# Optimization experiments

Hardware: AMD Instinct MI355X
Metric: run time of the kernel (lower is better)

## Reference

```python
import jax, jax.numpy as jnp
import numpy as np

BINARY_K = 64  # self.binary_k


def setup_inputs() -> dict:
    key = jax.random.key(0)
    ks = jax.random.split(key, 8)
    R, N, D, H = 8, 128, 512, 256
    obj_feats = jax.random.normal(ks[0], (R, N, D), dtype=jnp.float32)
    geo_feats = jax.random.normal(ks[1], (R, N, N, D), dtype=jnp.float32) * 0.1
    mask = jnp.ones((N, N), dtype=jnp.float32)
    mask = mask.at[jnp.arange(N), jnp.arange(N)].set(0.0)  # zero diagonal, as in forward()
    s1 = 1.0 / np.sqrt(D)
    s2 = 1.0 / np.sqrt(H)
    return {
        "obj_feats": obj_feats,
        "geo_feats": geo_feats,
        "mask": mask,
        "w1a": jax.random.normal(ks[2], (D, H), dtype=jnp.float32) * s1,
        "b1a": jnp.zeros((H,), dtype=jnp.float32),
        "w2a": jax.random.normal(ks[3], (H, 1), dtype=jnp.float32) * s2,
        "b2a": jnp.zeros((1,), dtype=jnp.float32),
        "w1b": jax.random.normal(ks[4], (D, H), dtype=jnp.float32) * s1,
        "b1b": jnp.zeros((H,), dtype=jnp.float32),
        "w2b": jax.random.normal(ks[5], (H, 1), dtype=jnp.float32) * s2,
        "b2b": jnp.zeros((1,), dtype=jnp.float32),
    }


def reference(obj_feats, geo_feats, mask, w1a, b1a, w2a, b2a, w1b, b1b, w2b, b2b):
    # pair_aware_perbatch (dropout = identity in eval mode)
    R, N, D = obj_feats.shape
    k = min(BINARY_K, N * N)

    # pairwise outer-product features + geometric features: [R, N, N, D]
    obj2obj = obj_feats[:, None, :, :] * obj_feats[:, :, None, :] + geo_feats

    # re_clf1 MLP scorer: D -> D/2 -> 1
    h = jax.nn.relu(jnp.einsum('rijd,dh->rijh', obj2obj, w1a) + b1a)
    logits = jnp.einsum('rijh,h->rij', h, w2a[:, 0]) + b2a[0]     # [R, N, N]
    o2o_logits = logits.reshape(R, N * N).sum(axis=0) / R          # [N*N]

    pair_probs = jax.nn.sigmoid(o2o_logits) * mask.ravel()
    _, topk_inds = jax.lax.top_k(pair_probs, k)                    # [k]

    # averaged pair features, gather topk
    a_obj2obj = obj2obj.reshape(R, N * N, D).sum(axis=0) / R       # [N*N, D]
    pair_feats = a_obj2obj[topk_inds]                              # [k, D]

    # pair-of-pair outer product + second MLP scorer
    p2p = pair_feats[None, :, :] * pair_feats[:, None, :]          # [k, k, D]
    h2 = jax.nn.relu(jnp.einsum('ijd,dh->ijh', p2p, w1b) + b1b)
    p2p_logits = jnp.einsum('ijh,h->ij', h2, w2b[:, 0]) + b2b[0]   # [k, k]

    return o2o_logits.reshape(N, N), p2p_logits, topk_inds
```

## Files before the change

### kernel.cpp

```cpp
#include <hip/hip_runtime.h>
#include <math.h>

typedef unsigned int u32;
typedef unsigned long long u64;
typedef unsigned short u16;
typedef short bf16x8 __attribute__((ext_vector_type(8)));
typedef float f32x4 __attribute__((ext_vector_type(4)));

#define RR 8
#define NN 128
#define DD 512
#define HH 256
#define KTOP 64
#define NCAND 256
#define NSEL 128

#define WS_LOGITS_OFF 0
#define WS_CAND_OFF   65536
#define WS_EXACT_OFF  66560
#define WS_CNT_OFF    67584
#define WS_TOPK_OFF   67600
#define WS_PF_OFF     67856
#define WS_WH_OFF     198928
#define WS_WL_OFF     461072

__device__ __forceinline__ u16 bf16rne(float x) {
    union { float f; u32 u; } v; v.f = x;
    u32 r = (v.u + 0x7fffu + ((v.u >> 16) & 1u)) >> 16;
    return (u16)r;
}
__device__ __forceinline__ float bf16tof(u16 h) {
    union { float f; u32 u; } v; v.u = ((u32)h) << 16; return v.f;
}
__device__ __forceinline__ u32 f32sort(float x) {
    union { float f; u32 u; } v; v.f = x;
    return v.u ^ ((v.u & 0x80000000u) ? 0xFFFFFFFFu : 0x80000000u);
}

__global__ __launch_bounds__(256) void k0_splitW(const float* __restrict__ W1,
                                                 u16* __restrict__ wh, u16* __restrict__ wl)
{
    const int kc = blockIdx.x;
    const int h  = threadIdx.x;
    const int swz = (h >> 1) & 3;
    u16 rh[32], rl[32];
#pragma unroll
    for (int kk = 0; kk < 32; ++kk) {
        float a = W1[(size_t)(kc * 32 + kk) * HH + h];
        u16 hi = bf16rne(a);
        float lo = a - bf16tof(hi);
        rh[kk] = hi; rl[kk] = bf16rne(lo);
    }
    const size_t base = (size_t)kc * 8192 + (size_t)h * 32;
#pragma unroll
    for (int q = 0; q < 4; ++q) {
        uint4 ph, pl;
        ph.x = (u32)rh[q*8+0] | ((u32)rh[q*8+1] << 16);
        ph.y = (u32)rh[q*8+2] | ((u32)rh[q*8+3] << 16);
        ph.z = (u32)rh[q*8+4] | ((u32)rh[q*8+5] << 16);
        ph.w = (u32)rh[q*8+6] | ((u32)rh[q*8+7] << 16);
        pl.x = (u32)rl[q*8+0] | ((u32)rl[q*8+1] << 16);
        pl.y = (u32)rl[q*8+2] | ((u32)rl[q*8+3] << 16);
        pl.z = (u32)rl[q*8+4] | ((u32)rl[q*8+5] << 16);
        pl.w = (u32)rl[q*8+6] | ((u32)rl[q*8+7] << 16);
        const int qs = (q ^ swz) * 8;
        *(uint4*)&wh[base + qs] = ph;
        *(uint4*)&wl[base + qs] = pl;
    }
}

__global__ __launch_bounds__(256, 2) void k1_pair_mfma(
    const float* __restrict__ obj, const float* __restrict__ geo,
    const u16* __restrict__ wh, const u16* __restrict__ wl,
    const float* __restrict__ b1, const float* __restrict__ w2,
    float* __restrict__ logits_acc)
{
    const int jb = blockIdx.x, i = blockIdx.y, r = blockIdx.z;
    const int j0 = jb * 64;
    const int tid = threadIdx.x;
    const int lane = tid & 63, wv = tid >> 6;
    const int l15 = lane & 15, quad = lane >> 4;
    const int fsl = (quad ^ ((l15 >> 1) & 3)) * 8;

    __shared__ float sObjI[DD];
    __shared__ __align__(16) u16 sAh[64 * 32], sAl[64 * 32];
    __shared__ __align__(16) u16 sBh[256 * 32], sBl[256 * 32];

    const float* objI = obj + (size_t)(r * NN + i) * DD;
    for (int t = tid; t < DD; t += 256) sObjI[t] = objI[t];

    f32x4 acc[4][4];
#pragma unroll
    for (int mt = 0; mt < 4; ++mt)
#pragma unroll
        for (int nt = 0; nt < 4; ++nt) acc[mt][nt] = (f32x4){0.f, 0.f, 0.f, 0.f};

    const float* geoB = geo + ((size_t)(r * NN + i) * NN + j0) * DD;
    const float* objJ = obj + (size_t)(r * NN + j0) * DD;

    const int aj = tid >> 2;
    const int ak = (tid & 3) * 8;
    const int asl = ((tid & 3) ^ ((aj >> 1) & 3)) * 8;

    for (int kc = 0; kc < 16; ++kc) {
        const int k0 = kc * 32;
        __syncthreads();
        {
            const char* gh = (const char*)(wh + (size_t)kc * 8192);
            const char* gl = (const char*)(wl + (size_t)kc * 8192);
#pragma unroll
            for (int p = 0; p < 4; ++p) {
                const int off = (wv * 4 + p) * 1024;
                __builtin_amdgcn_global_load_lds(
                    (const __attribute__((address_space(1))) u32*)(gh + off + lane * 16),
                    (__attribute__((address_space(3))) u32*)((char*)sBh + off), 16, 0, 0);
                __builtin_amdgcn_global_load_lds(
                    (const __attribute__((address_space(1))) u32*)(gl + off + lane * 16),
                    (__attribute__((address_space(3))) u32*)((char*)sBl + off), 16, 0, 0);
            }
        }
        {
            float4 g0 = *(const float4*)(geoB + (size_t)aj * DD + k0 + ak);
            float4 g1 = *(const float4*)(geoB + (size_t)aj * DD + k0 + ak + 4);
            float4 o0 = *(const float4*)(objJ + (size_t)aj * DD + k0 + ak);
            float4 o1 = *(const float4*)(objJ + (size_t)aj * DD + k0 + ak + 4);
            float a[8];
            a[0] = fmaf(sObjI[k0+ak+0], o0.x, g0.x);
            a[1] = fmaf(sObjI[k0+ak+1], o0.y, g0.y);
            a[2] = fmaf(sObjI[k0+ak+2], o0.z, g0.z);
            a[3] = fmaf(sObjI[k0+ak+3], o0.w, g0.w);
            a[4] = fmaf(sObjI[k0+ak+4], o1.x, g1.x);
            a[5] = fmaf(sObjI[k0+ak+5], o1.y, g1.y);
            a[6] = fmaf(sObjI[k0+ak+6], o1.z, g1.z);
            a[7] = fmaf(sObjI[k0+ak+7], o1.w, g1.w);
            u16 hs[8], ls[8];
#pragma unroll
            for (int q = 0; q < 8; ++q) {
                hs[q] = bf16rne(a[q]);
                ls[q] = bf16rne(a[q] - bf16tof(hs[q]));
            }
            uint4 ph, pl;
            ph.x = (u32)hs[0] | ((u32)hs[1] << 16); ph.y = (u32)hs[2] | ((u32)hs[3] << 16);
            ph.z = (u32)hs[4] | ((u32)hs[5] << 16); ph.w = (u32)hs[6] | ((u32)hs[7] << 16);
            pl.x = (u32)ls[0] | ((u32)ls[1] << 16); pl.y = (u32)ls[2] | ((u32)ls[3] << 16);
            pl.z = (u32)ls[4] | ((u32)ls[5] << 16); pl.w = (u32)ls[6] | ((u32)ls[7] << 16);
            *(uint4*)&sAh[aj * 32 + asl] = ph;
            *(uint4*)&sAl[aj * 32 + asl] = pl;
        }
        __syncthreads();
        bf16x8 Bh[4], Bl[4], Ah[4], Al[4];
#pragma unroll
        for (int nt = 0; nt < 4; ++nt) {
            const int row = wv * 64 + nt * 16 + l15;
            Bh[nt] = *(const bf16x8*)&sBh[row * 32 + fsl];
            Bl[nt] = *(const bf16x8*)&sBl[row * 32 + fsl];
        }
#pragma unroll
        for (int mt = 0; mt < 4; ++mt) {
            const int row = mt * 16 + l15;
            Ah[mt] = *(const bf16x8*)&sAh[row * 32 + fsl];
            Al[mt] = *(const bf16x8*)&sAl[row * 32 + fsl];
        }
#pragma unroll
        for (int mt = 0; mt < 4; ++mt)
#pragma unroll
            for (int nt = 0; nt < 4; ++nt) {
                acc[mt][nt] = __builtin_amdgcn_mfma_f32_16x16x32_bf16(Ah[mt], Bh[nt], acc[mt][nt], 0, 0, 0);
                acc[mt][nt] = __builtin_amdgcn_mfma_f32_16x16x32_bf16(Ah[mt], Bl[nt], acc[mt][nt], 0, 0, 0);
                acc[mt][nt] = __builtin_amdgcn_mfma_f32_16x16x32_bf16(Al[mt], Bh[nt], acc[mt][nt], 0, 0, 0);
            }
    }
    float pr[4][4];
#pragma unroll
    for (int mt = 0; mt < 4; ++mt)
#pragma unroll
        for (int t = 0; t < 4; ++t) pr[mt][t] = 0.f;
#pragma unroll
    for (int nt = 0; nt < 4; ++nt) {
        const int h = wv * 64 + nt * 16 + l15;
        const float bb = b1[h], w = w2[h];
#pragma unroll
        for (int mt = 0; mt < 4; ++mt)
#pragma unroll
            for (int t = 0; t < 4; ++t)
                pr[mt][t] += fmaxf(acc[mt][nt][t] + bb, 0.f) * w;
    }
#pragma unroll
    for (int mt = 0; mt < 4; ++mt)
#pragma unroll
        for (int t = 0; t < 4; ++t) {
            float v = pr[mt][t];
            v += __shfl_xor(v, 1); v += __shfl_xor(v, 2);
            v += __shfl_xor(v, 4); v += __shfl_xor(v, 8);
            if (l15 == 0)
                atomicAdd(&logits_acc[i * NN + j0 + mt * 16 + quad * 4 + t], v);
        }
}

__global__ __launch_bounds__(1024) void k2_hist(
    const float* __restrict__ logits_acc, const float* __restrict__ mask,
    const float* __restrict__ b2a, float* __restrict__ out,
    int* __restrict__ cand, int* __restrict__ cnt_out)
{
    __shared__ u32 hist[16 * 256];
    __shared__ u32 sum1[256];
    __shared__ int sB1, sRem, sT16;
    __shared__ u32 sCnt;
    const int t = threadIdx.x;
    const int hb = (t >> 6) << 8;
    for (int b = t; b < 16 * 256; b += 1024) hist[b] = 0;
    if (t == 0) sCnt = 0;
    __syncthreads();
    const float bias = b2a[0];
    u32 skey[16];
#pragma unroll
    for (int e = 0; e < 16; ++e) {
        const int idx = e * 1024 + t;
        const float lg = logits_acc[idx] * 0.125f + bias;
        out[idx] = lg;
        u32 s = f32sort(lg);
        if (mask[idx] == 0.f) s = 0;
        skey[e] = s;
        atomicAdd(&hist[hb + (s >> 24)], 1u);
    }
    __syncthreads();
    if (t < 256) {
        u32 s = 0;
#pragma unroll
        for (int c = 0; c < 16; ++c) s += hist[c * 256 + t];
        sum1[t] = s;
    }
    __syncthreads();
    if (t == 0) {
        u32 cum = 0; int b = 255;
        for (; b > 0; --b) { u32 c = sum1[b]; if (cum + c >= (u32)NSEL) break; cum += c; }
        sB1 = b; sRem = NSEL - (int)cum;
    }
    __syncthreads();
    const int B1 = sB1;
    for (int b = t; b < 16 * 256; b += 1024) hist[b] = 0;
    __syncthreads();
#pragma unroll
    for (int e = 0; e < 16; ++e) {
        const u32 s = skey[e];
        if ((int)(s >> 24) == B1) atomicAdd(&hist[hb + ((s >> 16) & 0xFF)], 1u);
    }
    __syncthreads();
    if (t < 256) {
        u32 s = 0;
#pragma unroll
        for (int c = 0; c < 16; ++c) s += hist[c * 256 + t];
        sum1[t] = s;
    }
    __syncthreads();
    if (t == 0) {
        const int rem = sRem; u32 cum = 0; int b = 255;
        for (; b > 0; --b) { cum += sum1[b]; if ((int)cum >= rem) break; }
        sT16 = (B1 << 8) | b;
    }
    __syncthreads();
    const u32 T16 = (u32)sT16;
#pragma unroll
    for (int e = 0; e < 16; ++e) {
        const u32 s = skey[e];
        if (s != 0 && (s >> 16) >= T16) {
            const u32 pos = atomicAdd(&sCnt, 1u);
            if (pos < (u32)NCAND) cand[pos] = e * 1024 + t;
        }
    }
    __syncthreads();
    if (t == 0) *cnt_out = (int)(sCnt < (u32)NCAND ? sCnt : (u32)NCAND);
}

__global__ __launch_bounds__(256) void k5_exact(
    const float* __restrict__ obj, const float* __restrict__ geo,
    const float* __restrict__ W1, const float* __restrict__ b1,
    const float* __restrict__ w2, const float* __restrict__ b2a,
    const int* __restrict__ cand, const int* __restrict__ cnt_ptr,
    float* __restrict__ exact)
{
    const int c = blockIdx.x;
    if (c >= *cnt_ptr) { if (threadIdx.x == 0) exact[c] = -1e30f; return; }
    const int idx = cand[c];
    const int i = idx >> 7, j = idx & 127;
    const int t = threadIdx.x;
    __shared__ float sA[RR][DD];
    __shared__ float sRed[4];
    for (int f = t; f < RR * DD; f += 256) {
        const int r = f >> 9, k = f & 511;
        sA[r][k] = fmaf(obj[(size_t)(r * NN + i) * DD + k],
                        obj[(size_t)(r * NN + j) * DD + k],
                        geo[((size_t)(r * NN + i) * NN + j) * DD + k]);
    }
    __syncthreads();
    float hv[RR];
#pragma unroll
    for (int r = 0; r < RR; ++r) hv[r] = 0.f;
#pragma unroll 4
    for (int k = 0; k < DD; ++k) {
        const float w = W1[(size_t)k * HH + t];
#pragma unroll
        for (int r = 0; r < RR; ++r) hv[r] = fmaf(sA[r][k], w, hv[r]);
    }
    const float bb = b1[t], wv2 = w2[t];
    float p = 0.f;
#pragma unroll
    for (int r = 0; r < RR; ++r) p += fmaxf(hv[r] + bb, 0.f) * wv2;
#pragma unroll
    for (int off = 1; off < 64; off <<= 1) p += __shfl_xor(p, off);
    if ((t & 63) == 0) sRed[t >> 6] = p;
    __syncthreads();
    if (t == 0) exact[c] = (sRed[0] + sRed[1] + sRed[2] + sRed[3]) * 0.125f + b2a[0];
}

__global__ __launch_bounds__(256) void k_sort(
    const float* __restrict__ exact, const int* __restrict__ cand,
    float* __restrict__ out, int* __restrict__ topk)
{
    __shared__ u64 sKey[NCAND];
    const int t = threadIdx.x;
    {
        const float lg = exact[t];
        u32 ps = 0; u32 idx = 0x7FFFFFFFu;
        if (lg > -1e29f) {
            const float p = 1.f / (1.f + expf(-lg));
            ps = f32sort(p);
            idx = (u32)cand[t];
        }
        sKey[t] = ((u64)ps << 32) | (u64)(0xFFFFFFFFu - idx);
    }
    for (int k = 2; k <= NCAND; k <<= 1)
        for (int j = k >> 1; j > 0; j >>= 1) {
            __syncthreads();
            const int ixj = t ^ j;
            if (ixj > t) {
                const u64 a = sKey[t], b = sKey[ixj];
                if (((t & k) == 0) ? (a < b) : (a > b)) { sKey[t] = b; sKey[ixj] = a; }
            }
        }
    __syncthreads();
    if (t < KTOP) {
        const u32 idx = 0xFFFFFFFFu - (u32)(sKey[t] & 0xFFFFFFFFull);
        topk[t] = (int)idx;
        out[20480 + t] = (float)idx;
    }
}

__global__ __launch_bounds__(256) void k3_gather(
    const float* __restrict__ obj, const float* __restrict__ geo,
    const int* __restrict__ ws_topk, float* __restrict__ pf)
{
    const int tix = blockIdx.x;
    const int idx = ws_topk[tix];
    const int i = idx >> 7, j = idx & 127;
    for (int dd = threadIdx.x; dd < DD; dd += 256) {
        float s = 0.f;
#pragma unroll
        for (int r = 0; r < RR; ++r) {
            const float oi = obj[(size_t)(r * NN + i) * DD + dd];
            const float oj = obj[(size_t)(r * NN + j) * DD + dd];
            const float g  = geo[((size_t)(r * NN + i) * NN + j) * DD + dd];
            s += oi * oj + g;
        }
        pf[tix * DD + dd] = s * 0.125f;
    }
}

__global__ __launch_bounds__(256) void k4_p2p(
    const float* __restrict__ pf, const float* __restrict__ W1,
    const float* __restrict__ b1, const float* __restrict__ w2,
    const float* __restrict__ b2, float* __restrict__ out)
{
    const int a = blockIdx.x;
    const int tid = threadIdx.x;
    const int tx = tid & 15, ty = tid >> 4;

    __shared__ float sPfA[DD];
    __shared__ __align__(16) float sA[32][68];
    __shared__ __align__(16) float sB[32][HH];

    const float* pfA = pf + (size_t)a * DD;
    for (int t = tid; t < DD; t += 256) sPfA[t] = pfA[t];

    float acc[4][16];
#pragma unroll
    for (int m = 0; m < 4; ++m)
#pragma unroll
        for (int n = 0; n < 16; ++n) acc[m][n] = 0.f;

    for (int kc = 0; kc < 16; ++kc) {
        const int k0 = kc * 32;
        __syncthreads();
#pragma unroll
        for (int p = 0; p < 8; ++p) {
            const int f = tid + p * 256;
            const int kk = f >> 6, c = (f & 63) << 2;
            *(float4*)&sB[kk][c] = *(const float4*)&W1[(size_t)(k0 + kk) * HH + c];
        }
#pragma unroll
        for (int p = 0; p < 2; ++p) {
            const int f = tid + p * 256;
            const int j = f >> 3, kk = (f & 7) << 2;
            float4 o = *(const float4*)(pf + (size_t)j * DD + k0 + kk);
            sA[kk + 0][j] = sPfA[k0 + kk + 0] * o.x;
            sA[kk + 1][j] = sPfA[k0 + kk + 1] * o.y;
            sA[kk + 2][j] = sPfA[k0 + kk + 2] * o.z;
            sA[kk + 3][j] = sPfA[k0 + kk + 3] * o.w;
        }
        __syncthreads();
#pragma unroll 8
        for (int kk = 0; kk < 32; ++kk) {
            float4 a4 = *(const float4*)&sA[kk][ty << 2];
            float av[4] = {a4.x, a4.y, a4.z, a4.w};
#pragma unroll
            for (int n4 = 0; n4 < 4; ++n4) {
                float4 b4 = *(const float4*)&sB[kk][(n4 << 6) + (tx << 2)];
                float bv[4] = {b4.x, b4.y, b4.z, b4.w};
#pragma unroll
                for (int m = 0; m < 4; ++m)
#pragma unroll
                    for (int c = 0; c < 4; ++c)
                        acc[m][(n4 << 2) + c] = fmaf(av[m], bv[c], acc[m][(n4 << 2) + c]);
            }
        }
    }
    const float b20 = b2[0];
    float pr[4] = {0.f, 0.f, 0.f, 0.f};
#pragma unroll
    for (int n4 = 0; n4 < 4; ++n4)
#pragma unroll
        for (int c = 0; c < 4; ++c) {
            const int h = (n4 << 6) + (tx << 2) + c;
            const float bb = b1[h], w = w2[h];
#pragma unroll
            for (int m = 0; m < 4; ++m)
                pr[m] += fmaxf(acc[m][(n4 << 2) + c] + bb, 0.f) * w;
        }
#pragma unroll
    for (int m = 0; m < 4; ++m) {
        pr[m] += __shfl_xor(pr[m], 1); pr[m] += __shfl_xor(pr[m], 2);
        pr[m] += __shfl_xor(pr[m], 4); pr[m] += __shfl_xor(pr[m], 8);
        if (tx == 0)
            out[16384 + a * 64 + (ty << 2) + m] = pr[m] + b20;
    }
}

extern "C" void kernel_launch(void* const* d_in, const int* in_sizes, int n_in,
                              void* d_out, int out_size, void* d_ws, size_t ws_size,
                              hipStream_t stream) {
    const float* obj  = (const float*)d_in[0];
    const float* geo  = (const float*)d_in[1];
    const float* mask = (const float*)d_in[2];
    const float* w1a  = (const float*)d_in[3];
    const float* b1a  = (const float*)d_in[4];
    const float* w2a  = (const float*)d_in[5];
    const float* b2a  = (const float*)d_in[6];
    const float* w1b  = (const float*)d_in[7];
    const float* b1b  = (const float*)d_in[8];
    const float* w2b  = (const float*)d_in[9];
    const float* b2b  = (const float*)d_in[10];
    float* out = (float*)d_out;

    char* ws = (char*)d_ws;
    float* ws_logits = (float*)(ws + WS_LOGITS_OFF);
    int*   ws_cand   = (int*)  (ws + WS_CAND_OFF);
    float* ws_exact  = (float*)(ws + WS_EXACT_OFF);
    int*   ws_cnt    = (int*)  (ws + WS_CNT_OFF);
    int*   ws_topk   = (int*)  (ws + WS_TOPK_OFF);
    float* ws_pf     = (float*)(ws + WS_PF_OFF);
    u16*   ws_wh     = (u16*)  (ws + WS_WH_OFF);
    u16*   ws_wl     = (u16*)  (ws + WS_WL_OFF);

    hipMemsetAsync(ws_logits, 0, 16384 * sizeof(float), stream);

    k0_splitW<<<16, 256, 0, stream>>>(w1a, ws_wh, ws_wl);
    k1_pair_mfma<<<dim3(2, NN, RR), 256, 0, stream>>>(obj, geo, ws_wh, ws_wl, b1a, w2a, ws_logits);
    k2_hist<<<1, 1024, 0, stream>>>(ws_logits, mask, b2a, out, ws_cand, ws_cnt);
    k5_exact<<<NCAND, 256, 0, stream>>>(obj, geo, w1a, b1a, w2a, b2a, ws_cand, ws_cnt, ws_exact);
    k_sort<<<1, 256, 0, stream>>>(ws_exact, ws_cand, out, ws_topk);
    k3_gather<<<KTOP, 256, 0, stream>>>(obj, geo, ws_topk, ws_pf);
    k4_p2p<<<KTOP, 256, 0, stream>>>(ws_pf, w1b, b1b, w2b, b2b, out);
}
```

Before: 636.8 us.

## Port p2p scorer to split-bf16 MFMA, fuse sort with gather, fold memset

The second MLP GEMM (k4_p2p) moves from FP32 FMA tiles to bf16 MFMA using a hi/lo split (four MFMAs per tile) to keep near-fp32 accuracy. W1b is split into hi/lo inside the kernel on every chunk. The single-block sort is merged with the top-k gather: each of 64 blocks redundantly sorts and then gathers its own row, which removes one launch. The logits memset is folded into an extra block of the weight-split kernel, and an unroll factor in k5_exact is raised. Together these cut launch count and FMA-bound GEMM time, at the cost of redundant sort work and repeated weight conversion in every block.

```diff
diff --git a/kernel.cpp b/kernel.cpp
--- a/kernel.cpp
+++ b/kernel.cpp
@@ -38,8 +38,15 @@
 }
 
 __global__ __launch_bounds__(256) void k0_splitW(const float* __restrict__ W1,
-                                                 u16* __restrict__ wh, u16* __restrict__ wl)
+                                                 u16* __restrict__ wh, u16* __restrict__ wl,
+                                                 float* __restrict__ logits)
 {
+    if (blockIdx.x == 16) {
+        float4 z = {0.f, 0.f, 0.f, 0.f};
+        for (int t = threadIdx.x; t < 4096; t += 256)
+            ((float4*)logits)[t] = z;
+        return;
+    }
     const int kc = blockIdx.x;
     const int h  = threadIdx.x;
     const int swz = (h >> 1) & 3;
@@ -296,7 +303,7 @@
     float hv[RR];
 #pragma unroll
     for (int r = 0; r < RR; ++r) hv[r] = 0.f;
-#pragma unroll 4
+#pragma unroll 8
     for (int k = 0; k < DD; ++k) {
         const float w = W1[(size_t)k * HH + t];
 #pragma unroll
@@ -313,9 +320,10 @@
     if (t == 0) exact[c] = (sRed[0] + sRed[1] + sRed[2] + sRed[3]) * 0.125f + b2a[0];
 }
 
-__global__ __launch_bounds__(256) void k_sort(
+__global__ __launch_bounds__(256) void k_sortgather(
     const float* __restrict__ exact, const int* __restrict__ cand,
-    float* __restrict__ out, int* __restrict__ topk)
+    const float* __restrict__ obj, const float* __restrict__ geo,
+    float* __restrict__ out, float* __restrict__ pf)
 {
     __shared__ u64 sKey[NCAND];
     const int t = threadIdx.x;
@@ -339,21 +347,14 @@
             }
         }
     __syncthreads();
-    if (t < KTOP) {
-        const u32 idx = 0xFFFFFFFFu - (u32)(sKey[t] & 0xFFFFFFFFull);
-        topk[t] = (int)idx;
-        out[20480 + t] = (float)idx;
-    }
-}
-
-__global__ __launch_bounds__(256) void k3_gather(
-    const float* __restrict__ obj, const float* __restrict__ geo,
-    const int* __restrict__ ws_topk, float* __restrict__ pf)
-{
     const int tix = blockIdx.x;
-    const int idx = ws_topk[tix];
+    if (tix == 0 && t < KTOP) {
+        const u32 oidx = 0xFFFFFFFFu - (u32)(sKey[t] & 0xFFFFFFFFull);
+        out[20480 + t] = (float)oidx;
+    }
+    const int idx = (int)(0xFFFFFFFFu - (u32)(sKey[tix] & 0xFFFFFFFFull));
     const int i = idx >> 7, j = idx & 127;
-    for (int dd = threadIdx.x; dd < DD; dd += 256) {
+    for (int dd = t; dd < DD; dd += 256) {
         float s = 0.f;
 #pragma unroll
         for (int r = 0; r < RR; ++r) {
@@ -373,76 +374,131 @@
 {
     const int a = blockIdx.x;
     const int tid = threadIdx.x;
-    const int tx = tid & 15, ty = tid >> 4;
+    const int lane = tid & 63, wv = tid >> 6;
+    const int l15 = lane & 15, quad = lane >> 4;
+    const int fsl = (quad ^ ((l15 >> 1) & 3)) * 8;
 
     __shared__ float sPfA[DD];
-    __shared__ __align__(16) float sA[32][68];
-    __shared__ __align__(16) float sB[32][HH];
+    __shared__ __align__(16) u16 sAh[64 * 32], sAl[64 * 32];
+    __shared__ __align__(16) u16 sBh[256 * 32], sBl[256 * 32];
+    __shared__ float sRed[4][64];
 
     const float* pfA = pf + (size_t)a * DD;
     for (int t = tid; t < DD; t += 256) sPfA[t] = pfA[t];
 
-    float acc[4][16];
-#pragma unroll
-    for (int m = 0; m < 4; ++m)
-#pragma unroll
-        for (int n = 0; n < 16; ++n) acc[m][n] = 0.f;
+    f32x4 acc[4][4];
+#pragma unroll
+    for (int mt = 0; mt < 4; ++mt)
+#pragma unroll
+        for (int nt = 0; nt < 4; ++nt) acc[mt][nt] = (f32x4){0.f, 0.f, 0.f, 0.f};
+
+    const int aj = tid >> 2;
+    const int ak = (tid & 3) * 8;
+    const int asl = ((tid & 3) ^ ((aj >> 1) & 3)) * 8;
+    const int swzB = (tid >> 1) & 3;
 
     for (int kc = 0; kc < 16; ++kc) {
         const int k0 = kc * 32;
         __syncthreads();
-#pragma unroll
-        for (int p = 0; p < 8; ++p) {
-            const int f = tid + p * 256;
-            const int kk = f >> 6, c = (f & 63) << 2;
-            *(float4*)&sB[kk][c] = *(const float4*)&W1[(size_t)(k0 + kk) * HH + c];
-        }
-#pragma unroll
-        for (int p = 0; p < 2; ++p) {
-            const int f = tid + p * 256;
-            const int j = f >> 3, kk = (f & 7) << 2;
-            float4 o = *(const float4*)(pf + (size_t)j * DD + k0 + kk);
-            sA[kk + 0][j] = sPfA[k0 + kk + 0] * o.x;
-            sA[kk + 1][j] = sPfA[k0 + kk + 1] * o.y;
-            sA[kk + 2][j] = sPfA[k0 + kk + 2] * o.z;
-            sA[kk + 3][j] = sPfA[k0 + kk + 3] * o.w;
+        {
+            u16 rh[32], rl[32];
+#pragma unroll
+            for (int kk = 0; kk < 32; ++kk) {
+                float w = W1[(size_t)(k0 + kk) * HH + tid];
+                u16 hi = bf16rne(w);
+                rh[kk] = hi; rl[kk] = bf16rne(w - bf16tof(hi));
+            }
+#pragma unroll
+            for (int q = 0; q < 4; ++q) {
+                uint4 ph, pl;
+                ph.x = (u32)rh[q*8+0] | ((u32)rh[q*8+1] << 16);
+                ph.y = (u32)rh[q*8+2] | ((u32)rh[q*8+3] << 16);
+                ph.z = (u32)rh[q*8+4] | ((u32)rh[q*8+5] << 16);
+                ph.w = (u32)rh[q*8+6] | ((u32)rh[q*8+7] << 16);
+                pl.x = (u32)rl[q*8+0] | ((u32)rl[q*8+1] << 16);
+                pl.y = (u32)rl[q*8+2] | ((u32)rl[q*8+3] << 16);
+                pl.z = (u32)rl[q*8+4] | ((u32)rl[q*8+5] << 16);
+                pl.w = (u32)rl[q*8+6] | ((u32)rl[q*8+7] << 16);
+                const int qs = (q ^ swzB) * 8;
+                *(uint4*)&sBh[tid * 32 + qs] = ph;
+                *(uint4*)&sBl[tid * 32 + qs] = pl;
+            }
+        }
+        {
+            float4 p0 = *(const float4*)(pf + (size_t)aj * DD + k0 + ak);
+            float4 p1 = *(const float4*)(pf + (size_t)aj * DD + k0 + ak + 4);
+            float av[8];
+            av[0] = sPfA[k0+ak+0] * p0.x; av[1] = sPfA[k0+ak+1] * p0.y;
+            av[2] = sPfA[k0+ak+2] * p0.z; av[3] = sPfA[k0+ak+3] * p0.w;
+            av[4] = sPfA[k0+ak+4] * p1.x; av[5] = sPfA[k0+ak+5] * p1.y;
+            av[6] = sPfA[k0+ak+6] * p1.z; av[7] = sPfA[k0+ak+7] * p1.w;
+            u16 hs[8], ls[8];
+#pragma unroll
+            for (int q = 0; q < 8; ++q) {
+                hs[q] = bf16rne(av[q]);
+                ls[q] = bf16rne(av[q] - bf16tof(hs[q]));
+            }
+            uint4 ph, pl;
+            ph.x = (u32)hs[0] | ((u32)hs[1] << 16); ph.y = (u32)hs[2] | ((u32)hs[3] << 16);
+            ph.z = (u32)hs[4] | ((u32)hs[5] << 16); ph.w = (u32)hs[6] | ((u32)hs[7] << 16);
+            pl.x = (u32)ls[0] | ((u32)ls[1] << 16); pl.y = (u32)ls[2] | ((u32)ls[3] << 16);
+            pl.z = (u32)ls[4] | ((u32)ls[5] << 16); pl.w = (u32)ls[6] | ((u32)ls[7] << 16);
+            *(uint4*)&sAh[aj * 32 + asl] = ph;
+            *(uint4*)&sAl[aj * 32 + asl] = pl;
         }
         __syncthreads();
-#pragma unroll 8
-        for (int kk = 0; kk < 32; ++kk) {
-            float4 a4 = *(const float4*)&sA[kk][ty << 2];
-            float av[4] = {a4.x, a4.y, a4.z, a4.w};
-#pragma unroll
-            for (int n4 = 0; n4 < 4; ++n4) {
-                float4 b4 = *(const float4*)&sB[kk][(n4 << 6) + (tx << 2)];
-                float bv[4] = {b4.x, b4.y, b4.z, b4.w};
-#pragma unroll
-                for (int m = 0; m < 4; ++m)
-#pragma unroll
-                    for (int c = 0; c < 4; ++c)
-                        acc[m][(n4 << 2) + c] = fmaf(av[m], bv[c], acc[m][(n4 << 2) + c]);
-            }
-        }
-    }
-    const float b20 = b2[0];
-    float pr[4] = {0.f, 0.f, 0.f, 0.f};
-#pragma unroll
-    for (int n4 = 0; n4 < 4; ++n4)
-#pragma unroll
-        for (int c = 0; c < 4; ++c) {
-            const int h = (n4 << 6) + (tx << 2) + c;
-            const float bb = b1[h], w = w2[h];
-#pragma unroll
-            for (int m = 0; m < 4; ++m)
-                pr[m] += fmaxf(acc[m][(n4 << 2) + c] + bb, 0.f) * w;
-        }
-#pragma unroll
-    for (int m = 0; m < 4; ++m) {
-        pr[m] += __shfl_xor(pr[m], 1); pr[m] += __shfl_xor(pr[m], 2);
-        pr[m] += __shfl_xor(pr[m], 4); pr[m] += __shfl_xor(pr[m], 8);
-        if (tx == 0)
-            out[16384 + a * 64 + (ty << 2) + m] = pr[m] + b20;
-    }
+        bf16x8 Bh[4], Bl[4], Ah[4], Al[4];
+#pragma unroll
+        for (int nt = 0; nt < 4; ++nt) {
+            const int row = wv * 64 + nt * 16 + l15;
+            Bh[nt] = *(const bf16x8*)&sBh[row * 32 + fsl];
+            Bl[nt] = *(const bf16x8*)&sBl[row * 32 + fsl];
+        }
+#pragma unroll
+        for (int mt = 0; mt < 4; ++mt) {
+            const int row = mt * 16 + l15;
+            Ah[mt] = *(const bf16x8*)&sAh[row * 32 + fsl];
+            Al[mt] = *(const bf16x8*)&sAl[row * 32 + fsl];
+        }
+#pragma unroll
+        for (int mt = 0; mt < 4; ++mt)
+#pragma unroll
+            for (int nt = 0; nt < 4; ++nt) {
+                acc[mt][nt] = __builtin_amdgcn_mfma_f32_16x16x32_bf16(Ah[mt], Bh[nt], acc[mt][nt], 0, 0, 0);
+                acc[mt][nt] = __builtin_amdgcn_mfma_f32_16x16x32_bf16(Ah[mt], Bl[nt], acc[mt][nt], 0, 0, 0);
+                acc[mt][nt] = __builtin_amdgcn_mfma_f32_16x16x32_bf16(Al[mt], Bh[nt], acc[mt][nt], 0, 0, 0);
+                acc[mt][nt] = __builtin_amdgcn_mfma_f32_16x16x32_bf16(Al[mt], Bl[nt], acc[mt][nt], 0, 0, 0);
+            }
+    }
+    float pr[4][4];
+#pragma unroll
+    for (int mt = 0; mt < 4; ++mt)
+#pragma unroll
+        for (int t = 0; t < 4; ++t) pr[mt][t] = 0.f;
+#pragma unroll
+    for (int nt = 0; nt < 4; ++nt) {
+        const int h = wv * 64 + nt * 16 + l15;
+        const float bb = b1[h], w = w2[h];
+#pragma unroll
+        for (int mt = 0; mt < 4; ++mt)
+#pragma unroll
+            for (int t = 0; t < 4; ++t)
+                pr[mt][t] += fmaxf(acc[mt][nt][t] + bb, 0.f) * w;
+    }
+#pragma unroll
+    for (int mt = 0; mt < 4; ++mt)
+#pragma unroll
+        for (int t = 0; t < 4; ++t) {
+            float v = pr[mt][t];
+            v += __shfl_xor(v, 1); v += __shfl_xor(v, 2);
+            v += __shfl_xor(v, 4); v += __shfl_xor(v, 8);
+            if (l15 == 0)
+                sRed[wv][mt * 16 + quad * 4 + t] = v;
+        }
+    __syncthreads();
+    if (tid < 64)
+        out[16384 + a * 64 + tid] =
+            sRed[0][tid] + sRed[1][tid] + sRed[2][tid] + sRed[3][tid] + b2[0];
 }
 
 extern "C" void kernel_launch(void* const* d_in, const int* in_sizes, int n_in,
@@ -466,18 +522,14 @@
     int*   ws_cand   = (int*)  (ws + WS_CAND_OFF);
     float* ws_exact  = (float*)(ws + WS_EXACT_OFF);
     int*   ws_cnt    = (int*)  (ws + WS_CNT_OFF);
-    int*   ws_topk   = (int*)  (ws + WS_TOPK_OFF);
     float* ws_pf     = (float*)(ws + WS_PF_OFF);
     u16*   ws_wh     = (u16*)  (ws + WS_WH_OFF);
     u16*   ws_wl     = (u16*)  (ws + WS_WL_OFF);
 
-    hipMemsetAsync(ws_logits, 0, 16384 * sizeof(float), stream);
-
-    k0_splitW<<<16, 256, 0, stream>>>(w1a, ws_wh, ws_wl);
+    k0_splitW<<<17, 256, 0, stream>>>(w1a, ws_wh, ws_wl, ws_logits);
     k1_pair_mfma<<<dim3(2, NN, RR), 256, 0, stream>>>(obj, geo, ws_wh, ws_wl, b1a, w2a, ws_logits);
     k2_hist<<<1, 1024, 0, stream>>>(ws_logits, mask, b2a, out, ws_cand, ws_cnt);
     k5_exact<<<NCAND, 256, 0, stream>>>(obj, geo, w1a, b1a, w2a, b2a, ws_cand, ws_cnt, ws_exact);
-    k_sort<<<1, 256, 0, stream>>>(ws_exact, ws_cand, out, ws_topk);
-    k3_gather<<<KTOP, 256, 0, stream>>>(obj, geo, ws_topk, ws_pf);
+    k_sortgather<<<KTOP, 256, 0, stream>>>(ws_exact, ws_cand, obj, geo, out, ws_pf);
     k4_p2p<<<KTOP, 256, 0, stream>>>(ws_pf, w1b, b1b, w2b, b2b, out);
 }
```

Result: faster. 546.0 us (-14.2%).
